# Performance work log

Hardware: AMD Instinct MI355X
Metric: run time of the kernel (lower is better)

## Reference

```python
import jax, jax.numpy as jnp
import numpy as np

B, T, P, D = 32, 8, 196, 768
M = 10
NUM_CLASSES = 100
NUM_IDX = 98
P_MASK = 0.5


def setup_inputs() -> dict:
    key = jax.random.key(0)
    ks = jax.random.split(key, 16)
    s = 0.02
    inp = {
        'visual': jax.random.normal(ks[0], (B, T * P, D), jnp.float32),
        'audio': jax.random.normal(ks[1], (B, D), jnp.float32),
        'causal': jax.random.normal(ks[2], (B, M, D), jnp.float32),
        'random_mask': jax.random.uniform(ks[3], (B, T, P, D)) < P_MASK,
        'Wa': jax.random.normal(ks[4], (D, D), jnp.float32) * s,
        'ba': jnp.zeros((D,), jnp.float32),
        'Wv': jax.random.normal(ks[5], (D, D), jnp.float32) * s,
        'bv': jnp.zeros((D,), jnp.float32),
        'Waa': jax.random.normal(ks[6], (D, D), jnp.float32) * s,
        'baa': jnp.zeros((D,), jnp.float32),
        'Wav': jax.random.normal(ks[7], (D, D), jnp.float32) * s,
        'bav': jnp.zeros((D,), jnp.float32),
        'Wf': jax.random.normal(ks[8], (D, D), jnp.float32) * s,
        'bf': jnp.zeros((D,), jnp.float32),
        'Wf2': jax.random.normal(ks[9], (D, 1), jnp.float32) * s,
        'bf2': jnp.zeros((1,), jnp.float32),
        'Wc': jax.random.normal(ks[10], (D, NUM_CLASSES), jnp.float32) * s,
        'bc': jnp.zeros((NUM_CLASSES,), jnp.float32),
        'causal_param': jnp.zeros((1,), jnp.float32),
    }
    return inp


def reference(visual, audio, causal, random_mask, Wa, ba, Wv, bv, Waa, baa,
              Wav, bav, Wf, bf, Wf2, bf2, Wc, bc, causal_param):
    vis = visual.reshape(visual.shape[0], T, -1, D)  # [B,8,196,768]

    # causal_intervention_mean_feature4
    cp = jax.nn.sigmoid(causal_param)                 # soft_clamp2, [1]
    feats = causal @ Wf + bf                          # [B,M,D]
    feats2 = jnp.swapaxes(causal @ Wf2 + bf2, 1, 2)   # [B,1,M]
    fw = jax.nn.softmax(jnp.tanh(feats), axis=1)      # [B,M,D]
    ci = jnp.einsum('bom,bmd->bd', feats2, fw * causal)  # bmm + squeeze
    audio2 = cp * ci + audio                          # [B,D]

    # audio_visual_attention1
    pa = jnp.tanh(audio2 @ Waa + baa)                 # [B,D]
    pv = jnp.tanh(vis @ Wav + bav)                    # [B,T,P,D]
    sscore = pv * pa[:, None, None, :]                # einsum ijkd,id->ijkd
    sattn = jax.nn.softmax(sscore, axis=2)            # softmax over patches
    patch = jnp.sum(sattn, axis=-1)                   # [B,T,P]
    thresh = jnp.sort(patch, axis=-1)[:, :, NUM_IDX]  # per (b,t) threshold
    spa_mask = patch < thresh[:, :, None]             # [B,T,P]
    final_mask = ~(spa_mask[..., None] & random_mask) # [B,T,P,D]
    sfilt = jnp.where(final_mask, sattn, 0.0)

    sav = jnp.sum(sfilt * pv, axis=2)                 # [B,T,D]
    tattn = jax.nn.softmax(sav * pa[:, None, :], axis=1)

    vp = jnp.sum(sfilt * vis, axis=2)                 # [B,T,D]
    vp = jnp.sum(tattn * vp, axis=1)                  # [B,D]

    af = jax.nn.relu(audio2 @ Wa + ba)
    vf = jax.nn.relu(vp @ Wv + bv)
    logits = (af + vf) @ Wc + bc                      # [B,num_classes]
    return logits
```

## Files before the change

### kernel.cpp

```cpp
#include <hip/hip_runtime.h>
#include <hip/hip_bf16.h>
#include <hip/hip_fp16.h>
#include <math.h>

#define BB 32
#define TT 8
#define PP 196
#define DD 768
#define MM 10
#define NCLS 100
#define NIDX 98

typedef __attribute__((ext_vector_type(8))) short short8v;
typedef __attribute__((ext_vector_type(4))) float float4v;

__device__ __forceinline__ float fast_tanh(float x) {
    float e = __expf(2.0f * x);
    return 1.0f - 2.0f / (e + 1.0f);
}
__device__ __forceinline__ unsigned short f2bf(float x) {
    __hip_bfloat16 h = __float2bfloat16(x);
    return *(unsigned short*)&h;
}
__device__ __forceinline__ unsigned short f2h(float x) {
    __half h = __float2half(x);
    return *(unsigned short*)&h;
}
__device__ __forceinline__ float h2f(unsigned short u) {
    __half h = *(__half*)&u;
    return __half2float(h);
}

__global__ __launch_bounds__(256) void k_split_w(const float* __restrict__ W,
    unsigned short* __restrict__ ht, const unsigned int* __restrict__ rm,
    int* __restrict__ mode, float* __restrict__ colsum) {
    __shared__ float tile[32][33];
    int bid = blockIdx.y * 24 + blockIdx.x;
    for (int i = bid * 256 + threadIdx.x; i < BB * TT * DD; i += 24 * 24 * 256)
        colsum[i] = 0.f;
    if (bid == 0) {
        __shared__ int f_ni, f_nf;
        if (threadIdx.x == 0) { f_ni = 0; f_nf = 0; }
        __syncthreads();
        int ni = 0, nf = 0;
        for (int i = threadIdx.x; i < 16384; i += 256) {
            unsigned int x = rm[i];
            ni |= (x > 1u) ? 1 : 0;
            nf |= (x != 0u && x != 0x3F800000u) ? 1 : 0;
        }
        if (ni) atomicOr(&f_ni, 1);
        if (nf) atomicOr(&f_nf, 1);
        __syncthreads();
        if (threadIdx.x == 0) *mode = f_ni ? (f_nf ? 2 : 1) : 0;
        __syncthreads();
    }
    int bn = blockIdx.x * 32;
    int bk = blockIdx.y * 32;
    int tx = threadIdx.x & 31, ty = threadIdx.x >> 5;
    #pragma unroll
    for (int i = 0; i < 4; ++i)
        tile[ty + i * 8][tx] = W[(size_t)(bk + ty + i * 8) * DD + bn + tx];
    __syncthreads();
    #pragma unroll
    for (int i = 0; i < 4; ++i) {
        int n = bn + ty + i * 8, k = bk + tx;
        ht[(size_t)n * DD + k] = f2bf(tile[tx][ty + i * 8]);
    }
}

__global__ __launch_bounds__(768) void k_feats_partial(
    const float* __restrict__ causal, const float* __restrict__ Wf,
    const float* __restrict__ Wf2,
    float* __restrict__ pf, float* __restrict__ pf2) {
    int b = blockIdx.x, kc = blockIdx.y;
    int k0 = kc * 192;
    int t = threadIdx.x;
    __shared__ float cs[MM][192];
    __shared__ float red[MM][12];
    for (int i = t; i < MM * 192; i += 768)
        cs[i / 192][i % 192] = causal[((size_t)b * MM + i / 192) * DD + k0 + i % 192];
    __syncthreads();
    int wave = t >> 6, lane = t & 63;
    float w2v = (t < 192) ? Wf2[k0 + t] : 0.f;
    #pragma unroll
    for (int m = 0; m < MM; ++m) {
        float p = (t < 192) ? cs[m][t] * w2v : 0.f;
        #pragma unroll
        for (int o = 32; o > 0; o >>= 1) p += __shfl_down(p, o);
        if (lane == 0) red[m][wave] = p;
    }
    __syncthreads();
    if (t < MM) {
        float s = 0.f;
        #pragma unroll
        for (int wv = 0; wv < 3; ++wv) s += red[t][wv];
        pf2[(b * 4 + kc) * MM + t] = s;
    }
    float acc[MM];
    #pragma unroll
    for (int m = 0; m < MM; ++m) acc[m] = 0.f;
    #pragma unroll 4
    for (int k = 0; k < 192; ++k) {
        float wv = Wf[(size_t)(k0 + k) * DD + t];
        #pragma unroll
        for (int m = 0; m < MM; ++m) acc[m] = fmaf(cs[m][k], wv, acc[m]);
    }
    #pragma unroll
    for (int m = 0; m < MM; ++m)
        pf[(((size_t)b * 4 + kc) * MM + m) * DD + t] = acc[m];
}

__global__ __launch_bounds__(768) void k_audio2a(
    const float* __restrict__ causal, const float* __restrict__ audio,
    const float* __restrict__ pf, const float* __restrict__ pf2,
    const float* __restrict__ bf, const float* __restrict__ bf2,
    const float* __restrict__ cparam, float* __restrict__ a2) {
    int b = blockIdx.x;
    int t = threadIdx.x;
    float cp = 1.0f / (1.0f + __expf(-cparam[0]));
    float tf[MM], f2[MM];
    float mx = -1e30f;
    #pragma unroll
    for (int m = 0; m < MM; ++m) {
        float acc = bf[t];
        float s2 = bf2[0];
        #pragma unroll
        for (int kc = 0; kc < 4; ++kc) {
            acc += pf[(((size_t)b * 4 + kc) * MM + m) * DD + t];
            s2 += pf2[(b * 4 + kc) * MM + m];
        }
        tf[m] = fast_tanh(acc);
        f2[m] = s2;
        mx = fmaxf(mx, tf[m]);
    }
    float s = 0.f;
    #pragma unroll
    for (int m = 0; m < MM; ++m) { tf[m] = __expf(tf[m] - mx); s += tf[m]; }
    float inv = 1.0f / s;
    float ci = 0.f;
    #pragma unroll
    for (int m = 0; m < MM; ++m)
        ci += f2[m] * (tf[m] * inv) * causal[((size_t)b * MM + m) * DD + t];
    a2[(size_t)b * DD + t] = cp * ci + audio[(size_t)b * DD + t];
}

__global__ __launch_bounds__(256) void k_audio2b(
    const float* __restrict__ a2,
    const float* __restrict__ Waa, const float* __restrict__ baa,
    const float* __restrict__ Wa, const float* __restrict__ ba,
    float* __restrict__ pa, float* __restrict__ af) {
    __shared__ float a2s[16][DD + 4];
    int sel = blockIdx.y;
    const float* W = sel ? Wa : Waa;
    int t = threadIdx.x;
    int c = blockIdx.x * 32 + (t & 31);
    int slot = t >> 5;
    float bias = sel ? ba[c] : baa[c];
    #pragma unroll
    for (int g = 0; g < 2; ++g) {
        if (g) __syncthreads();
        for (int i = t; i < 16 * DD; i += 256)
            a2s[i / DD][i % DD] = a2[(size_t)(g * 16 + i / DD) * DD + i % DD];
        __syncthreads();
        float acc0 = 0.f, acc1 = 0.f;
        #pragma unroll 8
        for (int k = 0; k < DD; ++k) {
            float wv = W[(size_t)k * DD + c];
            acc0 = fmaf(a2s[slot][k], wv, acc0);
            acc1 = fmaf(a2s[slot + 8][k], wv, acc1);
        }
        int b0 = g * 16 + slot, b1 = b0 + 8;
        if (sel == 0) {
            pa[(size_t)b0 * DD + c] = fast_tanh(acc0 + bias);
            pa[(size_t)b1 * DD + c] = fast_tanh(acc1 + bias);
        } else {
            af[(size_t)b0 * DD + c] = fmaxf(acc0 + bias, 0.f);
            af[(size_t)b1 * DD + c] = fmaxf(acc1 + bias, 0.f);
        }
    }
}

__global__ __launch_bounds__(256, 4) void k_pv_mfma(
    const float* __restrict__ vis, const unsigned short* __restrict__ Wht,
    const float* __restrict__ bav, const float* __restrict__ pa,
    unsigned short* __restrict__ pvh, float* __restrict__ colsum)
{
    __shared__ unsigned short Ah[128 * 64];
    __shared__ unsigned short Bh[128 * 64];
    int wg = blockIdx.x;
    int lin = (wg & 7) * 294 + (wg >> 3);
    int mt = lin / 6, nt = lin % 6;
    int i0 = mt * 128, n0 = nt * 128;
    int t = threadIdx.x, w = t >> 6, l = t & 63;
    int wm = (w >> 1) * 64, wn = (w & 1) * 64;

    float4v zero4 = {0.f, 0.f, 0.f, 0.f};
    float4v acc[4][4];
    #pragma unroll
    for (int a = 0; a < 4; ++a)
        #pragma unroll
        for (int b = 0; b < 4; ++b) acc[a][b] = zero4;

    int brow[4], bcs[4];
    #pragma unroll
    for (int j = 0; j < 4; ++j) {
        int row = (w * 4 + j) * 8 + (l >> 3);
        brow[j] = row;
        bcs[j] = (l & 7) ^ (row & 7);
    }
    int arow = t >> 1, acb = (t & 1) * 4;
    const float* avbase = vis + (size_t)(i0 + arow) * DD + acb * 8;
    int aoff[4];
    #pragma unroll
    for (int c4 = 0; c4 < 4; ++c4) {
        int c = acb + c4;
        aoff[c4] = arow * 64 + ((c ^ (arow & 7)) * 8);
    }

    float f[32];
    #pragma unroll
    for (int q = 0; q < 8; ++q)
        *(float4*)&f[q * 4] = *(const float4*)(avbase + q * 4);

    for (int wnd = 0; wnd < 12; ++wnd) {
        __syncthreads();
        unsigned int hw[16];
        #pragma unroll
        for (int i = 0; i < 16; ++i) {
            float2 fp = make_float2(f[2 * i], f[2 * i + 1]);
            __hip_bfloat162 h2 = __float22bfloat162_rn(fp);
            hw[i] = *(unsigned int*)&h2;
        }
        #pragma unroll
        for (int c4 = 0; c4 < 4; ++c4)
            *(uint4*)&Ah[aoff[c4]] = *(const uint4*)&hw[c4 * 4];
        int kw = wnd * 64;
        #pragma unroll
        for (int j = 0; j < 4; ++j) {
            size_t off = (size_t)(n0 + brow[j]) * DD + kw + bcs[j] * 8;
            __builtin_amdgcn_global_load_lds(
                (const __attribute__((address_space(1))) unsigned int*)(Wht + off),
                (__attribute__((address_space(3))) unsigned int*)&Bh[(w * 4 + j) * 512],
                16, 0, 0);
        }
        __syncthreads();
        if (wnd < 11) {
            const float* ap = avbase + (wnd + 1) * 64;
            #pragma unroll
            for (int q = 0; q < 8; ++q)
                *(float4*)&f[q * 4] = *(const float4*)(ap + q * 4);
        }
        #pragma unroll
        for (int kk = 0; kk < 2; ++kk) {
            short8v ahf[4], bhf[4];
            #pragma unroll
            for (int mr = 0; mr < 4; ++mr) {
                int row = wm + mr * 16 + (l & 15);
                int c = kk * 4 + (l >> 4);
                ahf[mr] = *(const short8v*)&Ah[row * 64 + ((c ^ (row & 7)) * 8)];
            }
            #pragma unroll
            for (int nc = 0; nc < 4; ++nc) {
                int row = wn + nc * 16 + (l & 15);
                int c = kk * 4 + (l >> 4);
                bhf[nc] = *(const short8v*)&Bh[row * 64 + ((c ^ (row & 7)) * 8)];
            }
            #pragma unroll
            for (int mr = 0; mr < 4; ++mr)
                #pragma unroll
                for (int nc = 0; nc < 4; ++nc)
                    acc[mr][nc] = __builtin_amdgcn_mfma_f32_16x16x32_bf16(
                        ahf[mr], bhf[nc], acc[mr][nc], 0, 0, 0);
        }
    }
    float* cred = (float*)&Ah[0];
    __syncthreads();
    if (t < 256) cred[t] = 0.f;
    __syncthreads();
    int bt0 = i0 / PP;
    int btbound = (bt0 + 1) * PP;
    #pragma unroll
    for (int nc = 0; nc < 4; ++nc) {
        int cl = wn + nc * 16 + (l & 15);
        int col = n0 + cl;
        float bias = bav[col];
        #pragma unroll
        for (int mr = 0; mr < 4; ++mr) {
            int row0 = i0 + wm + mr * 16 + ((l >> 4) << 2);
            int bq = row0 / (TT * PP);
            float pav = pa[(size_t)bq * DD + col];
            float esum = 0.f;
            #pragma unroll
            for (int v = 0; v < 4; ++v) {
                unsigned short pb = f2h(fast_tanh(acc[mr][nc][v] + bias));
                pvh[(size_t)(row0 + v) * DD + col] = pb;
                esum += __expf(h2f(pb) * pav);
            }
            int btg = (row0 >= btbound) ? 1 : 0;
            atomicAdd(&cred[btg * 128 + cl], esum);
        }
    }
    __syncthreads();
    if (t < 256) {
        int btg = t >> 7, cl = t & 127;
        if (btg == 0 || btbound < i0 + 128)
            atomicAdd(&colsum[(size_t)(bt0 + btg) * DD + n0 + cl], cred[t]);
    }
}

__global__ __launch_bounds__(768) void k_spatial(
    const unsigned short* __restrict__ pvh, const float* __restrict__ vis,
    const void* __restrict__ rmask, const int* __restrict__ mode_p,
    const float* __restrict__ pa, const float* __restrict__ colsum,
    float* __restrict__ sav, float* __restrict__ vpt) {
    int bt = blockIdx.x;
    int b = bt >> 3;
    size_t base = (size_t)bt * PP * DD;
    __shared__ float2 pi[DD];
    __shared__ float patch[PP];
    __shared__ unsigned char spa[PP];
    int t = threadIdx.x;
    float pav = pa[(size_t)b * DD + t];
    float inv = 1.0f / colsum[(size_t)bt * DD + t];
    pi[t] = make_float2(pav, inv);
    __syncthreads();
    int wave = t >> 6, lane = t & 63;
    for (int p = wave; p < PP; p += 12) {
        const uint2* rv = (const uint2*)(pvh + base + (size_t)p * DD);
        float sum = 0.f;
        #pragma unroll
        for (int j = lane; j < 192; j += 64) {
            uint2 v = rv[j];
            int c = j * 4;
            float2 q0 = pi[c], q1 = pi[c + 1], q2 = pi[c + 2], q3 = pi[c + 3];
            sum += __expf(h2f((unsigned short)(v.x & 0xFFFFu)) * q0.x) * q0.y
                 + __expf(h2f((unsigned short)(v.x >> 16)) * q1.x) * q1.y
                 + __expf(h2f((unsigned short)(v.y & 0xFFFFu)) * q2.x) * q2.y
                 + __expf(h2f((unsigned short)(v.y >> 16)) * q3.x) * q3.y;
        }
        #pragma unroll
        for (int o = 32; o > 0; o >>= 1) sum += __shfl_down(sum, o);
        if (lane == 0) patch[p] = sum;
    }
    __syncthreads();
    if (t < PP) {
        float x = patch[t];
        int c = 0;
        for (int q = 0; q < PP; ++q) c += (patch[q] <= x) ? 1 : 0;
        spa[t] = (c <= NIDX) ? 1 : 0;
    }
    __syncthreads();
    int mode = *mode_p;
    const unsigned short* pvb = pvh + base + t;
    const float* visb = vis + base + t;
    float sava = 0.f, vpa = 0.f;
    if (mode == 0) {
        const int* mb = (const int*)rmask + base + t;
        #pragma unroll 8
        for (int p = 0; p < PP; ++p) {
            float pvv = h2f(pvb[(size_t)p * DD]);
            float sa = __expf(pvv * pav) * inv;
            bool km = !(spa[p] && (mb[(size_t)p * DD] != 0));
            if (km) { sava = fmaf(sa, pvv, sava); vpa = fmaf(sa, visb[(size_t)p * DD], vpa); }
        }
    } else if (mode == 1) {
        const float* mb = (const float*)rmask + base + t;
        #pragma unroll 8
        for (int p = 0; p < PP; ++p) {
            float pvv = h2f(pvb[(size_t)p * DD]);
            float sa = __expf(pvv * pav) * inv;
            bool km = !(spa[p] && (mb[(size_t)p * DD] != 0.f));
            if (km) { sava = fmaf(sa, pvv, sava); vpa = fmaf(sa, visb[(size_t)p * DD], vpa); }
        }
    } else {
        const unsigned char* mb = (const unsigned char*)rmask + base + t;
        #pragma unroll 8
        for (int p = 0; p < PP; ++p) {
            float pvv = h2f(pvb[(size_t)p * DD]);
            float sa = __expf(pvv * pav) * inv;
            bool km = !(spa[p] && (mb[(size_t)p * DD] != 0));
            if (km) { sava = fmaf(sa, pvv, sava); vpa = fmaf(sa, visb[(size_t)p * DD], vpa); }
        }
    }
    sav[(size_t)bt * DD + t] = sava;
    vpt[(size_t)bt * DD + t] = vpa;
}

__global__ __launch_bounds__(768) void k_tail_a(
    const float* __restrict__ sav, const float* __restrict__ vpt,
    const float* __restrict__ pa, float* __restrict__ vp) {
    int b = blockIdx.x;
    int t = threadIdx.x;
    float pav = pa[(size_t)b * DD + t];
    float x[TT];
    float mx = -1e30f;
    #pragma unroll
    for (int k = 0; k < TT; ++k) {
        x[k] = sav[((size_t)b * TT + k) * DD + t] * pav;
        mx = fmaxf(mx, x[k]);
    }
    float s = 0.f;
    #pragma unroll
    for (int k = 0; k < TT; ++k) { x[k] = __expf(x[k] - mx); s += x[k]; }
    float inv = 1.0f / s;
    float acc = 0.f;
    #pragma unroll
    for (int k = 0; k < TT; ++k)
        acc += x[k] * inv * vpt[((size_t)b * TT + k) * DD + t];
    vp[(size_t)b * DD + t] = acc;
}

__global__ __launch_bounds__(256) void k_tail_b(
    const float* __restrict__ vp, const float* __restrict__ af,
    const float* __restrict__ Wv, const float* __restrict__ bv,
    float* __restrict__ h) {
    __shared__ float vs[16][DD + 4];
    int t = threadIdx.x;
    int c = blockIdx.x * 32 + (t & 31);
    int slot = t >> 5;
    float bias = bv[c];
    #pragma unroll
    for (int g = 0; g < 2; ++g) {
        if (g) __syncthreads();
        for (int i = t; i < 16 * DD; i += 256)
            vs[i / DD][i % DD] = vp[(size_t)(g * 16 + i / DD) * DD + i % DD];
        __syncthreads();
        float acc0 = 0.f, acc1 = 0.f;
        #pragma unroll 8
        for (int k = 0; k < DD; ++k) {
            float wv = Wv[(size_t)k * DD + c];
            acc0 = fmaf(vs[slot][k], wv, acc0);
            acc1 = fmaf(vs[slot + 8][k], wv, acc1);
        }
        int b0 = g * 16 + slot, b1 = b0 + 8;
        h[(size_t)b0 * DD + c] = fmaxf(acc0 + bias, 0.f) + af[(size_t)b0 * DD + c];
        h[(size_t)b1 * DD + c] = fmaxf(acc1 + bias, 0.f) + af[(size_t)b1 * DD + c];
    }
}

__global__ __launch_bounds__(256) void k_tail_c(
    const float* __restrict__ h, const float* __restrict__ Wc,
    const float* __restrict__ bc, float* __restrict__ out) {
    int t = threadIdx.x;
    int c = blockIdx.x * 8 + (t & 7);
    int b = t >> 3;
    if (c >= NCLS) return;
    float acc = bc[c];
    #pragma unroll 8
    for (int k = 0; k < DD; ++k)
        acc = fmaf(h[(size_t)b * DD + k], Wc[(size_t)k * NCLS + c], acc);
    out[(size_t)b * NCLS + c] = acc;
}

extern "C" void kernel_launch(void* const* d_in, const int* in_sizes, int n_in,
                              void* d_out, int out_size, void* d_ws, size_t ws_size,
                              hipStream_t stream) {
    const float* visual = (const float*)d_in[0];
    const float* audio  = (const float*)d_in[1];
    const float* causal = (const float*)d_in[2];
    const void*  rmask  = d_in[3];
    const float* Wa   = (const float*)d_in[4];
    const float* ba   = (const float*)d_in[5];
    const float* Wv   = (const float*)d_in[6];
    const float* bv   = (const float*)d_in[7];
    const float* Waa  = (const float*)d_in[8];
    const float* baa  = (const float*)d_in[9];
    const float* Wav  = (const float*)d_in[10];
    const float* bav  = (const float*)d_in[11];
    const float* Wf   = (const float*)d_in[12];
    const float* bf   = (const float*)d_in[13];
    const float* Wf2  = (const float*)d_in[14];
    const float* bf2  = (const float*)d_in[15];
    const float* Wc   = (const float*)d_in[16];
    const float* bc   = (const float*)d_in[17];
    const float* cpar = (const float*)d_in[18];
    float* out = (float*)d_out;

    unsigned short* Wht = (unsigned short*)d_ws;
    float* pf    = (float*)(Wht + (size_t)DD * DD);
    float* pf2   = pf + (size_t)BB * 4 * MM * DD;
    float* a2w   = pf2 + 2048;
    float* paw   = a2w + (size_t)BB * DD;
    float* afw   = paw + (size_t)BB * DD;
    float* colsum = afw + (size_t)BB * DD;
    unsigned short* pvh = (unsigned short*)(colsum + (size_t)BB * TT * DD);
    float* savw  = (float*)(pvh + (size_t)BB * TT * PP * DD);
    float* vptw  = savw + (size_t)BB * TT * DD;
    float* vpw   = vptw + (size_t)BB * TT * DD;
    float* hw    = vpw + (size_t)BB * DD;
    int*   modew = (int*)(hw + (size_t)BB * DD);

    k_split_w<<<dim3(24, 24), 256, 0, stream>>>(Wav, Wht, (const unsigned int*)rmask,
                                                modew, colsum);
    k_feats_partial<<<dim3(BB, 4), 768, 0, stream>>>(causal, Wf, Wf2, pf, pf2);
    k_audio2a<<<BB, 768, 0, stream>>>(causal, audio, pf, pf2, bf, bf2, cpar, a2w);
    k_audio2b<<<dim3(24, 2), 256, 0, stream>>>(a2w, Waa, baa, Wa, ba, paw, afw);
    k_pv_mfma<<<2352, 256, 0, stream>>>(visual, Wht, bav, paw, pvh, colsum);
    k_spatial<<<BB * TT, 768, 0, stream>>>(pvh, visual, rmask, modew, paw, colsum, savw, vptw);
    k_tail_a<<<BB, 768, 0, stream>>>(savw, vptw, paw, vpw);
    k_tail_b<<<24, 256, 0, stream>>>(vpw, afw, Wv, bv, hw);
    k_tail_c<<<13, 256, 0, stream>>>(hw, Wc, bc, out);
}
```

Before: 583.8 us.

## Pre-convert visual to bf16, async-load both GEMM operands, split spatial pass

```diff
diff --git a/kernel.cpp b/kernel.cpp
--- a/kernel.cpp
+++ b/kernel.cpp
@@ -22,6 +22,9 @@
     __hip_bfloat16 h = __float2bfloat16(x);
     return *(unsigned short*)&h;
 }
+__device__ __forceinline__ float bf2f(unsigned short h) {
+    return __uint_as_float(((unsigned)h) << 16);
+}
 __device__ __forceinline__ unsigned short f2h(float x) {
     __half h = __float2half(x);
     return *(unsigned short*)&h;
@@ -31,29 +34,44 @@
     return __half2float(h);
 }
 
-__global__ __launch_bounds__(256) void k_split_w(const float* __restrict__ W,
-    unsigned short* __restrict__ ht, const unsigned int* __restrict__ rm,
-    int* __restrict__ mode, float* __restrict__ colsum) {
-    __shared__ float tile[32][33];
-    int bid = blockIdx.y * 24 + blockIdx.x;
-    for (int i = bid * 256 + threadIdx.x; i < BB * TT * DD; i += 24 * 24 * 256)
-        colsum[i] = 0.f;
-    if (bid == 0) {
+__global__ __launch_bounds__(256) void k_prep(
+    const float* __restrict__ vis, unsigned short* __restrict__ visb,
+    const unsigned int* __restrict__ rm, int* __restrict__ mode) {
+    const size_t NC = (size_t)BB * TT * PP * DD / 8;
+    size_t gid = (size_t)blockIdx.x * 256 + threadIdx.x;
+    size_t nthr = (size_t)gridDim.x * 256;
+    for (size_t i = gid; i < NC; i += nthr) {
+        const float4* s = (const float4*)(vis + i * 8);
+        float4 x = s[0], y = s[1];
+        __hip_bfloat162 h;
+        unsigned int u0, u1, u2, u3;
+        h = __float22bfloat162_rn(make_float2(x.x, x.y)); u0 = *(unsigned int*)&h;
+        h = __float22bfloat162_rn(make_float2(x.z, x.w)); u1 = *(unsigned int*)&h;
+        h = __float22bfloat162_rn(make_float2(y.x, y.y)); u2 = *(unsigned int*)&h;
+        h = __float22bfloat162_rn(make_float2(y.z, y.w)); u3 = *(unsigned int*)&h;
+        uint4 o; o.x = u0; o.y = u1; o.z = u2; o.w = u3;
+        ((uint4*)visb)[i] = o;
+    }
+    if (blockIdx.x == 0) {
         __shared__ int f_ni, f_nf;
         if (threadIdx.x == 0) { f_ni = 0; f_nf = 0; }
         __syncthreads();
         int ni = 0, nf = 0;
         for (int i = threadIdx.x; i < 16384; i += 256) {
-            unsigned int x = rm[i];
-            ni |= (x > 1u) ? 1 : 0;
-            nf |= (x != 0u && x != 0x3F800000u) ? 1 : 0;
+            unsigned int v = rm[i];
+            ni |= (v > 1u) ? 1 : 0;
+            nf |= (v != 0u && v != 0x3F800000u) ? 1 : 0;
         }
         if (ni) atomicOr(&f_ni, 1);
         if (nf) atomicOr(&f_nf, 1);
         __syncthreads();
         if (threadIdx.x == 0) *mode = f_ni ? (f_nf ? 2 : 1) : 0;
-        __syncthreads();
-    }
+    }
+}
+
+__global__ __launch_bounds__(256) void k_split_w(const float* __restrict__ W,
+    unsigned short* __restrict__ ht) {
+    __shared__ float tile[32][33];
     int bn = blockIdx.x * 32;
     int bk = blockIdx.y * 32;
     int tx = threadIdx.x & 31, ty = threadIdx.x >> 5;
@@ -73,18 +91,18 @@
     const float* __restrict__ Wf2,
     float* __restrict__ pf, float* __restrict__ pf2) {
     int b = blockIdx.x, kc = blockIdx.y;
-    int k0 = kc * 192;
-    int t = threadIdx.x;
-    __shared__ float cs[MM][192];
+    int k0 = kc * 256;
+    int t = threadIdx.x;
+    __shared__ float cs[MM][256];
     __shared__ float red[MM][12];
-    for (int i = t; i < MM * 192; i += 768)
-        cs[i / 192][i % 192] = causal[((size_t)b * MM + i / 192) * DD + k0 + i % 192];
+    for (int i = t; i < MM * 256; i += 768)
+        cs[i >> 8][i & 255] = causal[((size_t)b * MM + (i >> 8)) * DD + k0 + (i & 255)];
     __syncthreads();
     int wave = t >> 6, lane = t & 63;
-    float w2v = (t < 192) ? Wf2[k0 + t] : 0.f;
+    float w2v = (t < 256) ? Wf2[k0 + t] : 0.f;
     #pragma unroll
     for (int m = 0; m < MM; ++m) {
-        float p = (t < 192) ? cs[m][t] * w2v : 0.f;
+        float p = (t < 256) ? cs[m][t] * w2v : 0.f;
         #pragma unroll
         for (int o = 32; o > 0; o >>= 1) p += __shfl_down(p, o);
         if (lane == 0) red[m][wave] = p;
@@ -93,21 +111,21 @@
     if (t < MM) {
         float s = 0.f;
         #pragma unroll
-        for (int wv = 0; wv < 3; ++wv) s += red[t][wv];
-        pf2[(b * 4 + kc) * MM + t] = s;
+        for (int wv = 0; wv < 4; ++wv) s += red[t][wv];
+        pf2[(b * 3 + kc) * MM + t] = s;
     }
     float acc[MM];
     #pragma unroll
     for (int m = 0; m < MM; ++m) acc[m] = 0.f;
     #pragma unroll 4
-    for (int k = 0; k < 192; ++k) {
+    for (int k = 0; k < 256; ++k) {
         float wv = Wf[(size_t)(k0 + k) * DD + t];
         #pragma unroll
         for (int m = 0; m < MM; ++m) acc[m] = fmaf(cs[m][k], wv, acc[m]);
     }
     #pragma unroll
     for (int m = 0; m < MM; ++m)
-        pf[(((size_t)b * 4 + kc) * MM + m) * DD + t] = acc[m];
+        pf[(((size_t)b * 3 + kc) * MM + m) * DD + t] = acc[m];
 }
 
 __global__ __launch_bounds__(768) void k_audio2a(
@@ -125,9 +143,9 @@
         float acc = bf[t];
         float s2 = bf2[0];
         #pragma unroll
-        for (int kc = 0; kc < 4; ++kc) {
-            acc += pf[(((size_t)b * 4 + kc) * MM + m) * DD + t];
-            s2 += pf2[(b * 4 + kc) * MM + m];
+        for (int kc = 0; kc < 3; ++kc) {
+            acc += pf[(((size_t)b * 3 + kc) * MM + m) * DD + t];
+            s2 += pf2[(b * 3 + kc) * MM + m];
         }
         tf[m] = fast_tanh(acc);
         f2[m] = s2;
@@ -148,7 +166,9 @@
     const float* __restrict__ a2,
     const float* __restrict__ Waa, const float* __restrict__ baa,
     const float* __restrict__ Wa, const float* __restrict__ ba,
-    float* __restrict__ pa, float* __restrict__ af) {
+    float* __restrict__ pa, float* __restrict__ af, float* __restrict__ colsum) {
+    int gid0 = (blockIdx.y * 24 + blockIdx.x) * 256 + threadIdx.x;
+    for (int i = gid0; i < BB * TT * DD; i += 48 * 256) colsum[i] = 0.f;
     __shared__ float a2s[16][DD + 4];
     int sel = blockIdx.y;
     const float* W = sel ? Wa : Waa;
@@ -180,13 +200,13 @@
     }
 }
 
-__global__ __launch_bounds__(256, 4) void k_pv_mfma(
-    const float* __restrict__ vis, const unsigned short* __restrict__ Wht,
+__global__ __launch_bounds__(256, 5) void k_pv_mfma(
+    const unsigned short* __restrict__ visb, const unsigned short* __restrict__ Wht,
     const float* __restrict__ bav, const float* __restrict__ pa,
     unsigned short* __restrict__ pvh, float* __restrict__ colsum)
 {
-    __shared__ unsigned short Ah[128 * 64];
-    __shared__ unsigned short Bh[128 * 64];
+    __shared__ unsigned short As[128 * 64];
+    __shared__ unsigned short Bs[128 * 64];
     int wg = blockIdx.x;
     int lin = (wg & 7) * 294 + (wg >> 3);
     int mt = lin / 6, nt = lin % 6;
@@ -208,48 +228,24 @@
         brow[j] = row;
         bcs[j] = (l & 7) ^ (row & 7);
     }
-    int arow = t >> 1, acb = (t & 1) * 4;
-    const float* avbase = vis + (size_t)(i0 + arow) * DD + acb * 8;
-    int aoff[4];
-    #pragma unroll
-    for (int c4 = 0; c4 < 4; ++c4) {
-        int c = acb + c4;
-        aoff[c4] = arow * 64 + ((c ^ (arow & 7)) * 8);
-    }
-
-    float f[32];
-    #pragma unroll
-    for (int q = 0; q < 8; ++q)
-        *(float4*)&f[q * 4] = *(const float4*)(avbase + q * 4);
 
     for (int wnd = 0; wnd < 12; ++wnd) {
         __syncthreads();
-        unsigned int hw[16];
-        #pragma unroll
-        for (int i = 0; i < 16; ++i) {
-            float2 fp = make_float2(f[2 * i], f[2 * i + 1]);
-            __hip_bfloat162 h2 = __float22bfloat162_rn(fp);
-            hw[i] = *(unsigned int*)&h2;
-        }
-        #pragma unroll
-        for (int c4 = 0; c4 < 4; ++c4)
-            *(uint4*)&Ah[aoff[c4]] = *(const uint4*)&hw[c4 * 4];
         int kw = wnd * 64;
         #pragma unroll
         for (int j = 0; j < 4; ++j) {
-            size_t off = (size_t)(n0 + brow[j]) * DD + kw + bcs[j] * 8;
+            size_t aoff = (size_t)(i0 + brow[j]) * DD + kw + bcs[j] * 8;
             __builtin_amdgcn_global_load_lds(
-                (const __attribute__((address_space(1))) unsigned int*)(Wht + off),
-                (__attribute__((address_space(3))) unsigned int*)&Bh[(w * 4 + j) * 512],
+                (const __attribute__((address_space(1))) unsigned int*)(visb + aoff),
+                (__attribute__((address_space(3))) unsigned int*)&As[(w * 4 + j) * 512],
                 16, 0, 0);
+            size_t boff = (size_t)(n0 + brow[j]) * DD + kw + bcs[j] * 8;
+            __builtin_amdgcn_global_load_lds(
+                (const __attribute__((address_space(1))) unsigned int*)(Wht + boff),
+                (__attribute__((address_space(3))) unsigned int*)&Bs[(w * 4 + j) * 512],
+                16, 0, 0);
         }
         __syncthreads();
-        if (wnd < 11) {
-            const float* ap = avbase + (wnd + 1) * 64;
-            #pragma unroll
-            for (int q = 0; q < 8; ++q)
-                *(float4*)&f[q * 4] = *(const float4*)(ap + q * 4);
-        }
         #pragma unroll
         for (int kk = 0; kk < 2; ++kk) {
             short8v ahf[4], bhf[4];
@@ -257,13 +253,13 @@
             for (int mr = 0; mr < 4; ++mr) {
                 int row = wm + mr * 16 + (l & 15);
                 int c = kk * 4 + (l >> 4);
-                ahf[mr] = *(const short8v*)&Ah[row * 64 + ((c ^ (row & 7)) * 8)];
+                ahf[mr] = *(const short8v*)&As[row * 64 + ((c ^ (row & 7)) * 8)];
             }
             #pragma unroll
             for (int nc = 0; nc < 4; ++nc) {
                 int row = wn + nc * 16 + (l & 15);
                 int c = kk * 4 + (l >> 4);
-                bhf[nc] = *(const short8v*)&Bh[row * 64 + ((c ^ (row & 7)) * 8)];
+                bhf[nc] = *(const short8v*)&Bs[row * 64 + ((c ^ (row & 7)) * 8)];
             }
             #pragma unroll
             for (int mr = 0; mr < 4; ++mr)
@@ -273,7 +269,7 @@
                         ahf[mr], bhf[nc], acc[mr][nc], 0, 0, 0);
         }
     }
-    float* cred = (float*)&Ah[0];
+    float* cred = (float*)&As[0];
     __syncthreads();
     if (t < 256) cred[t] = 0.f;
     __syncthreads();
@@ -308,17 +304,14 @@
     }
 }
 
-__global__ __launch_bounds__(768) void k_spatial(
-    const unsigned short* __restrict__ pvh, const float* __restrict__ vis,
-    const void* __restrict__ rmask, const int* __restrict__ mode_p,
-    const float* __restrict__ pa, const float* __restrict__ colsum,
-    float* __restrict__ sav, float* __restrict__ vpt) {
+__global__ __launch_bounds__(768) void k_patch(
+    const unsigned short* __restrict__ pvh, const float* __restrict__ pa,
+    const float* __restrict__ colsum, unsigned char* __restrict__ spa_g) {
     int bt = blockIdx.x;
     int b = bt >> 3;
     size_t base = (size_t)bt * PP * DD;
     __shared__ float2 pi[DD];
     __shared__ float patch[PP];
-    __shared__ unsigned char spa[PP];
     int t = threadIdx.x;
     float pav = pa[(size_t)b * DD + t];
     float inv = 1.0f / colsum[(size_t)bt * DD + t];
@@ -347,43 +340,72 @@
         float x = patch[t];
         int c = 0;
         for (int q = 0; q < PP; ++q) c += (patch[q] <= x) ? 1 : 0;
-        spa[t] = (c <= NIDX) ? 1 : 0;
-    }
-    __syncthreads();
+        spa_g[bt * PP + t] = (c <= NIDX) ? 1 : 0;
+    }
+}
+
+__global__ __launch_bounds__(768) void k_masked(
+    const unsigned short* __restrict__ pvh, const unsigned short* __restrict__ visb,
+    const void* __restrict__ rmask, const int* __restrict__ mode_p,
+    const float* __restrict__ pa, const float* __restrict__ colsum,
+    const unsigned char* __restrict__ spa_g,
+    float* __restrict__ sav, float* __restrict__ vpt) {
+    int bt = blockIdx.x;
+    int half = blockIdx.y;
+    int b = bt >> 3;
+    size_t base = (size_t)bt * PP * DD;
+    __shared__ unsigned char spa[PP];
+    __shared__ float red_s[2][384];
+    __shared__ float red_v[2][384];
+    int t = threadIdx.x;
+    if (t < PP) spa[t] = spa_g[bt * PP + t];
+    int pg = (t >= 384) ? 1 : 0;
+    int c = t - pg * 384;
+    int col = half * 384 + c;
+    int p0 = pg * 98, p1 = p0 + 98;
+    float pav = pa[(size_t)b * DD + col];
+    float inv = 1.0f / colsum[(size_t)bt * DD + col];
+    __syncthreads();
+    const unsigned short* pvb = pvh + base + col;
+    const unsigned short* vib = visb + base + col;
+    float sava = 0.f, vpa = 0.f;
     int mode = *mode_p;
-    const unsigned short* pvb = pvh + base + t;
-    const float* visb = vis + base + t;
-    float sava = 0.f, vpa = 0.f;
     if (mode == 0) {
-        const int* mb = (const int*)rmask + base + t;
-        #pragma unroll 8
-        for (int p = 0; p < PP; ++p) {
+        const int* mb = (const int*)rmask + base + col;
+        #pragma unroll 7
+        for (int p = p0; p < p1; ++p) {
             float pvv = h2f(pvb[(size_t)p * DD]);
             float sa = __expf(pvv * pav) * inv;
             bool km = !(spa[p] && (mb[(size_t)p * DD] != 0));
-            if (km) { sava = fmaf(sa, pvv, sava); vpa = fmaf(sa, visb[(size_t)p * DD], vpa); }
+            if (km) { sava = fmaf(sa, pvv, sava); vpa = fmaf(sa, bf2f(vib[(size_t)p * DD]), vpa); }
         }
     } else if (mode == 1) {
-        const float* mb = (const float*)rmask + base + t;
-        #pragma unroll 8
-        for (int p = 0; p < PP; ++p) {
+        const float* mb = (const float*)rmask + base + col;
+        #pragma unroll 7
+        for (int p = p0; p < p1; ++p) {
             float pvv = h2f(pvb[(size_t)p * DD]);
             float sa = __expf(pvv * pav) * inv;
             bool km = !(spa[p] && (mb[(size_t)p * DD] != 0.f));
-            if (km) { sava = fmaf(sa, pvv, sava); vpa = fmaf(sa, visb[(size_t)p * DD], vpa); }
+            if (km) { sava = fmaf(sa, pvv, sava); vpa = fmaf(sa, bf2f(vib[(size_t)p * DD]), vpa); }
         }
     } else {
-        const unsigned char* mb = (const unsigned char*)rmask + base + t;
-        #pragma unroll 8
-        for (int p = 0; p < PP; ++p) {
+        const unsigned char* mb = (const unsigned char*)rmask + base + col;
+        #pragma unroll 7
+        for (int p = p0; p < p1; ++p) {
             float pvv = h2f(pvb[(size_t)p * DD]);
             float sa = __expf(pvv * pav) * inv;
             bool km = !(spa[p] && (mb[(size_t)p * DD] != 0));
-            if (km) { sava = fmaf(sa, pvv, sava); vpa = fmaf(sa, visb[(size_t)p * DD], vpa); }
-        }
-    }
-    sav[(size_t)bt * DD + t] = sava;
-    vpt[(size_t)bt * DD + t] = vpa;
+            if (km) { sava = fmaf(sa, pvv, sava); vpa = fmaf(sa, bf2f(vib[(size_t)p * DD]), vpa); }
+        }
+    }
+    red_s[pg][c] = sava;
+    red_v[pg][c] = vpa;
+    __syncthreads();
+    if (t < 384) {
+        int col2 = half * 384 + t;
+        sav[(size_t)bt * DD + col2] = red_s[0][t] + red_s[1][t];
+        vpt[(size_t)bt * DD + col2] = red_v[0][t] + red_v[1][t];
+    }
 }
 
 __global__ __launch_bounds__(768) void k_tail_a(
@@ -476,27 +498,33 @@
     const float* cpar = (const float*)d_in[18];
     float* out = (float*)d_out;
 
+    const size_t NE = (size_t)BB * TT * PP * DD;
     unsigned short* Wht = (unsigned short*)d_ws;
-    float* pf    = (float*)(Wht + (size_t)DD * DD);
-    float* pf2   = pf + (size_t)BB * 4 * MM * DD;
-    float* a2w   = pf2 + 2048;
-    float* paw   = a2w + (size_t)BB * DD;
-    float* afw   = paw + (size_t)BB * DD;
-    float* colsum = afw + (size_t)BB * DD;
-    unsigned short* pvh = (unsigned short*)(colsum + (size_t)BB * TT * DD);
-    float* savw  = (float*)(pvh + (size_t)BB * TT * PP * DD);
+    float* pfreg = (float*)(Wht + (size_t)DD * DD);
+    float* colsum = pfreg;
+    float* savw  = colsum + (size_t)BB * TT * DD;
     float* vptw  = savw + (size_t)BB * TT * DD;
     float* vpw   = vptw + (size_t)BB * TT * DD;
     float* hw    = vpw + (size_t)BB * DD;
-    int*   modew = (int*)(hw + (size_t)BB * DD);
-
-    k_split_w<<<dim3(24, 24), 256, 0, stream>>>(Wav, Wht, (const unsigned int*)rmask,
-                                                modew, colsum);
-    k_feats_partial<<<dim3(BB, 4), 768, 0, stream>>>(causal, Wf, Wf2, pf, pf2);
+    unsigned char* spa_g = (unsigned char*)(hw + (size_t)BB * DD);
+    float* pf    = pfreg;
+    float* pf2   = pfreg + (size_t)BB * 3 * MM * DD;
+    float* a2w   = pf2 + 1024;
+    float* paw   = a2w + (size_t)BB * DD;
+    float* afw   = paw + (size_t)BB * DD;
+    int*   modew = (int*)(afw + (size_t)BB * DD);
+    unsigned short* visb = (unsigned short*)(modew + 16);
+    unsigned short* pvh  = visb + NE;
+
+    k_prep<<<2048, 256, 0, stream>>>(visual, visb, (const unsigned int*)rmask, modew);
+    k_split_w<<<dim3(24, 24), 256, 0, stream>>>(Wav, Wht);
+    k_feats_partial<<<dim3(BB, 3), 768, 0, stream>>>(causal, Wf, Wf2, pf, pf2);
     k_audio2a<<<BB, 768, 0, stream>>>(causal, audio, pf, pf2, bf, bf2, cpar, a2w);
-    k_audio2b<<<dim3(24, 2), 256, 0, stream>>>(a2w, Waa, baa, Wa, ba, paw, afw);
-    k_pv_mfma<<<2352, 256, 0, stream>>>(visual, Wht, bav, paw, pvh, colsum);
-    k_spatial<<<BB * TT, 768, 0, stream>>>(pvh, visual, rmask, modew, paw, colsum, savw, vptw);
+    k_audio2b<<<dim3(24, 2), 256, 0, stream>>>(a2w, Waa, baa, Wa, ba, paw, afw, colsum);
+    k_pv_mfma<<<2352, 256, 0, stream>>>(visb, Wht, bav, paw, pvh, colsum);
+    k_patch<<<BB * TT, 768, 0, stream>>>(pvh, paw, colsum, spa_g);
+    k_masked<<<dim3(BB * TT, 2), 768, 0, stream>>>(pvh, visb, rmask, modew, paw,
+                                                   colsum, spa_g, savw, vptw);
     k_tail_a<<<BB, 768, 0, stream>>>(savw, vptw, paw, vpw);
     k_tail_b<<<24, 256, 0, stream>>>(vpw, afw, Wv, bv, hw);
     k_tail_c<<<13, 256, 0, stream>>>(hw, Wc, bc, out);
```

New measurement: 532.7 us. 8.8% less time.
